# Performance work log

Hardware: AMD Instinct MI355X
Metric: run time of the kernel (lower is better)

## Reference

```python
import jax, jax.numpy as jnp
import numpy as np

DIM_IN, DIM_OUT, DIM_INNER = 1024, 1024, 128
SCALE = DIM_INNER ** -0.5


def setup_inputs() -> dict:
    key = jax.random.key(0)
    k1, k2, k3, k4 = jax.random.split(key, 4)
    x = jax.random.normal(k1, (4, 4096, DIM_IN), dtype=jnp.float32)
    # torch nn.Linear stores weight as [out, in]; we keep that layout and transpose in matmul
    w_qkv = jax.random.normal(k2, (3 * DIM_INNER, DIM_IN), dtype=jnp.float32) * (DIM_IN ** -0.5)
    w_out = jax.random.normal(k3, (DIM_OUT, DIM_INNER), dtype=jnp.float32) * (DIM_INNER ** -0.5)
    b_out = jax.random.normal(k4, (DIM_OUT,), dtype=jnp.float32) * 0.02
    return {"x": x, "w_qkv": w_qkv, "w_out": w_out, "b_out": b_out}


def reference(x, w_qkv, w_out, b_out):
    # qkv projection (no bias)
    qkv = jnp.einsum('bnd,ed->bne', x, w_qkv)            # [b, n, 3*dim_inner]
    q, k, v = jnp.split(qkv, 3, axis=-1)                 # each [b, n, dim_inner]
    sim = jnp.einsum('bid,bjd->bij', q, k) * SCALE       # [b, n, n]
    n = sim.shape[-1]
    causal = jnp.triu(jnp.ones((n, n), dtype=bool), 1)   # True above diagonal
    neg = jnp.finfo(q.dtype).max
    sim = jnp.where(causal[None, :, :], -neg, sim)
    attn = jax.nn.softmax(sim, axis=-1)
    out = jnp.einsum('bij,bjd->bid', attn, v)            # [b, n, dim_inner]
    return jnp.einsum('bnd,od->bno', out, w_out) + b_out # [b, n, dim_out]
```

## Files before the change

kernel.cpp:

```cpp
#include <hip/hip_runtime.h>
#include <math.h>


typedef __attribute__((ext_vector_type(8))) short bf16x8;
typedef __attribute__((ext_vector_type(4))) short bf16x4;
typedef __attribute__((ext_vector_type(4))) float f32x4;

#define FA_SCL2 0.12751886525137387f

__device__ __forceinline__ unsigned short f2bf(float f) {
    __bf16 h = (__bf16)f;
    return __builtin_bit_cast(unsigned short, h);
}
__device__ __forceinline__ float bf2f(unsigned short h) {
    union { unsigned u; float f; } v; v.u = ((unsigned)h) << 16;
    return v.f;
}
__device__ __forceinline__ f32x4 mfma16(bf16x8 a, bf16x8 b, f32x4 c) {
    return __builtin_amdgcn_mfma_f32_16x16x32_bf16(a, b, c, 0, 0, 0);
}
__device__ __forceinline__ void gl2lds16(const void* g, void* l) {
    __builtin_amdgcn_global_load_lds(
        (const __attribute__((address_space(1))) unsigned int*)g,
        (__attribute__((address_space(3))) unsigned int*)l, 16, 0, 0);
}
__device__ __forceinline__ f32x4 vmax4(f32x4 a, f32x4 b) {
    return f32x4{fmaxf(a[0], b[0]), fmaxf(a[1], b[1]),
                 fmaxf(a[2], b[2]), fmaxf(a[3], b[3])};
}

__global__ __launch_bounds__(256)
void wcast(const float* __restrict__ W, unsigned short* __restrict__ wfm)
{
    const int idx = blockIdx.x * 256 + threadIdx.x;
    const int kc = idx & 127, r = idx >> 7;
    const float* g = W + (size_t)r * 1024 + kc * 8;
    float4 w0 = *(const float4*)g, w1 = *(const float4*)(g + 4);
    bf16x8 p;
    p[0] = (short)f2bf(w0.x); p[1] = (short)f2bf(w0.y);
    p[2] = (short)f2bf(w0.z); p[3] = (short)f2bf(w0.w);
    p[4] = (short)f2bf(w1.x); p[5] = (short)f2bf(w1.y);
    p[6] = (short)f2bf(w1.z); p[7] = (short)f2bf(w1.w);
    *(bf16x8*)&wfm[(size_t)(kc * 384 + r) * 8] = p;
}

__global__ __launch_bounds__(256)
void woutcast(const float* __restrict__ W, unsigned short* __restrict__ wofm)
{
    const int idx = blockIdx.x * 256 + threadIdx.x;
    const int c = idx & 15, rg = idx >> 4;
    const float* g = W + (size_t)rg * 128 + c * 8;
    float4 w0 = *(const float4*)g, w1 = *(const float4*)(g + 4);
    bf16x8 p;
    p[0] = (short)f2bf(w0.x); p[1] = (short)f2bf(w0.y);
    p[2] = (short)f2bf(w0.z); p[3] = (short)f2bf(w0.w);
    p[4] = (short)f2bf(w1.x); p[5] = (short)f2bf(w1.y);
    p[6] = (short)f2bf(w1.z); p[7] = (short)f2bf(w1.w);
    *(bf16x8*)&wofm[((size_t)((rg >> 6) * 16 + c) * 64 + (rg & 63)) * 8] = p;
}

__global__ __launch_bounds__(256, 4)
void gemm_qkv(const float* __restrict__ X, const unsigned short* __restrict__ Wfm,
              unsigned short* __restrict__ qfm, unsigned short* __restrict__ kfm,
              unsigned short* __restrict__ vpl)
{
    __shared__ unsigned short Asl[2048];
    __shared__ unsigned short Bsl[3][6144];
    const int tid = threadIdx.x;
    const int wv = tid >> 6, lane = tid & 63;
    const int lm = lane & 15, quad = lane >> 4;
    const int mt = blockIdx.x & 255;
    const int nh = blockIdx.x >> 8;
    const int mb = mt * 64, nb = nh * 192;
    const int arow = tid >> 2, af4 = tid & 3;

    f32x4 acc[4][3];
    #pragma unroll
    for (int i = 0; i < 4; ++i)
        #pragma unroll
        for (int j = 0; j < 3; ++j) acc[i][j] = f32x4{0.f, 0.f, 0.f, 0.f};

    const float* gx = X + (size_t)(mb + arow) * 1024 + af4 * 8;

    auto issueB = [&](int it, int buf) {
        #pragma unroll
        for (int i = 0; i < 3; ++i) {
            const int p = wv * 3 + i;
            const int kcl = p & 3, rg = p >> 2;
            gl2lds16(Wfm + ((size_t)((it * 4 + kcl) * 384) + nb + rg * 64) * 8 + lane * 8,
                     &Bsl[buf][(kcl * 192 + rg * 64) * 8]);
        }
    };

    float4 a00 = *(const float4*)gx;
    float4 a01 = *(const float4*)(gx + 4);
    issueB(0, 0);
    float4 a10 = *(const float4*)(gx + 32);
    float4 a11 = *(const float4*)(gx + 36);
    issueB(1, 1);

    auto step = [&](const int i, float4& fa, float4& fb) {
        __builtin_amdgcn_s_barrier();
        {
            bf16x8 pk;
            pk[0] = (short)f2bf(fa.x); pk[1] = (short)f2bf(fa.y);
            pk[2] = (short)f2bf(fa.z); pk[3] = (short)f2bf(fa.w);
            pk[4] = (short)f2bf(fb.x); pk[5] = (short)f2bf(fb.y);
            pk[6] = (short)f2bf(fb.z); pk[7] = (short)f2bf(fb.w);
            *(bf16x8*)&Asl[(af4 * 64 + arow) * 8] = pk;
        }
        if (i < 30) {
            fa = *(const float4*)(gx + (i + 2) * 32);
            fb = *(const float4*)(gx + (i + 2) * 32 + 4);
            issueB(i + 2, (i + 2) % 3);
            asm volatile("s_waitcnt vmcnt(10) lgkmcnt(0)" ::: "memory");
        } else if (i == 30) {
            asm volatile("s_waitcnt vmcnt(5) lgkmcnt(0)" ::: "memory");
        } else {
            asm volatile("s_waitcnt vmcnt(0) lgkmcnt(0)" ::: "memory");
        }
        __builtin_amdgcn_s_barrier();
        const unsigned short* Bc = Bsl[i % 3];
        bf16x8 afr[4], bfr[3];
        #pragma unroll
        for (int i4 = 0; i4 < 4; ++i4)
            afr[i4] = *(const bf16x8*)&Asl[(quad * 64 + i4 * 16 + lm) * 8];
        #pragma unroll
        for (int j = 0; j < 3; ++j)
            bfr[j] = *(const bf16x8*)&Bc[(quad * 192 + wv * 48 + j * 16 + lm) * 8];
        #pragma unroll
        for (int i4 = 0; i4 < 4; ++i4)
            #pragma unroll
            for (int j = 0; j < 3; ++j)
                acc[i4][j] = mfma16(afr[i4], bfr[j], acc[i4][j]);
    };

    for (int p = 0; p < 16; ++p) { step(2 * p, a00, a01); step(2 * p + 1, a10, a11); }

    #pragma unroll
    for (int j = 0; j < 3; ++j) {
        const int ncg = nb + wv * 48 + j * 16 + lm;
        const int sect = ncg >> 7, ncol = ncg & 127;
        if (sect == 2) {
            #pragma unroll
            for (int i = 0; i < 4; ++i)
                #pragma unroll
                for (int r = 0; r < 4; ++r)
                    vpl[(size_t)(mb + i * 16 + quad * 4 + r) * 128 + ncol]
                        = f2bf(acc[i][j][r]);
        } else {
            unsigned short* dst = sect ? kfm : qfm;
            const float scl = sect ? 1.f : FA_SCL2;
            const size_t cb = ((size_t)mt * 16 + (ncol >> 3)) * 512 + (ncol & 7);
            #pragma unroll
            for (int i = 0; i < 4; ++i)
                #pragma unroll
                for (int r = 0; r < 4; ++r)
                    dst[cb + (size_t)(i * 16 + quad * 4 + r) * 8]
                        = f2bf(acc[i][j][r] * scl);
        }
    }
}

__global__ __launch_bounds__(256)
void transpose_v(const unsigned short* __restrict__ V, unsigned short* __restrict__ Vfm)
{
    __shared__ unsigned short T[128 * 72];
    const int tid = threadIdx.x;
    const int b  = blockIdx.x >> 6;
    const int kt = blockIdx.x & 63;
    const unsigned short* src = V + ((size_t)b * 4096 + kt * 64) * 128;
    #pragma unroll
    for (int i = 0; i < 4; ++i) {
        const int idx = tid + i * 256;
        const int key = idx >> 4, c8 = (idx & 15) * 8;
        bf16x8 d = *(const bf16x8*)(src + key * 128 + c8);
        #pragma unroll
        for (int e = 0; e < 8; ++e) T[(c8 + e) * 72 + key] = (unsigned short)d[e];
    }
    __syncthreads();
    unsigned short* dst = Vfm + (size_t)(b * 64 + kt) * 8192;
    #pragma unroll
    for (int i = 0; i < 4; ++i) {
        const int o = tid + i * 256;
        const int d = o & 127, c = o >> 7;
        bf16x8 x = *(const bf16x8*)&T[d * 72 + c * 8];
        *(bf16x8*)(dst + ((size_t)c * 128 + d) * 8) = x;
    }
}

__global__ __launch_bounds__(512, 4)
void flash_attn3(const unsigned short* __restrict__ Qfm, const unsigned short* __restrict__ Kfm,
                 const unsigned short* __restrict__ Vfm,
                 unsigned short* __restrict__ Opart, float* __restrict__ Ml)
{
    __shared__ unsigned short Klds[2][8192];
    __shared__ unsigned short Vlds[2][8192];
    __shared__ unsigned short Plds[8][1024];

    const int tid = threadIdx.x;
    const int wv = tid >> 6, lane = tid & 63;
    const int lm = lane & 15, quad = lane >> 4;

    const int bx = blockIdx.x;
    const int xcd = bx & 7;
    const int b   = xcd >> 1;
    const int r   = (bx >> 3) * 2 + (xcd & 1);
    const int sp  = r & 3;
    const int Qi  = (r < 64) ? (16 + (r >> 2)) : (15 - ((r - 64) >> 2));
    const int n   = 2 * Qi + 2;
    const int cnt = (n >> 2) + ((sp < (n & 3)) ? 1 : 0);
    const int ktb = sp * (n >> 2) + ((sp < (n & 3)) ? sp : (n & 3));
    const int kte = ktb + cnt;
    const int qtw = 2 * Qi + (wv >> 2);
    const int rw  = (wv & 3) * 16;

    const int qt0 = 2 * Qi;
    const size_t ob0 = (size_t)((b * 64 + qt0) * 4 + sp) * 8192;
    const size_t ob1 = ob0 + 4 * 8192;
    const int mlb0 = ((b * 64 + qt0) * 4 + sp) * 128, mlb1 = mlb0 + 512;

    if (cnt == 0) {
        bf16x8 z = {0, 0, 0, 0, 0, 0, 0, 0};
        #pragma unroll
        for (int t = 0; t < 2; ++t) {
            *(bf16x8*)&Opart[ob0 + (size_t)(tid + t * 512) * 8] = z;
            *(bf16x8*)&Opart[ob1 + (size_t)(tid + t * 512) * 8] = z;
        }
        if (tid < 64) { Ml[mlb0 + tid] = -INFINITY; Ml[mlb1 + tid] = -INFINITY; }
        else if (tid < 128) { Ml[mlb0 + tid] = 0.f; Ml[mlb1 + tid] = 0.f; }
        return;
    }

    {
        const size_t qb = (size_t)(b * 64 + qt0) * 8192;
        #pragma unroll
        for (int i = 0; i < 4; ++i) {
            const int p = wv * 4 + i;
            gl2lds16(Qfm + qb + (size_t)p * 512 + lane * 8, &Klds[0][0] + p * 512);
        }
    }
    __syncthreads();
    bf16x8 qf[4];
    {
        const unsigned short* Qt = &Klds[wv >> 2][0];
        #pragma unroll
        for (int c = 0; c < 4; ++c)
            qf[c] = *(const bf16x8*)&Qt[((c * 4 + quad) * 64 + rw + lm) * 8];
    }
    asm volatile("s_waitcnt lgkmcnt(0)" ::: "memory");
    __builtin_amdgcn_s_barrier();

    {
        const size_t kb = (size_t)(b * 64 + ktb) * 8192;
        #pragma unroll
        for (int i = 0; i < 2; ++i) {
            const int pc = wv * 2 + i;
            gl2lds16(Kfm + kb + pc * 512 + lane * 8, &Klds[0][pc * 512]);
            gl2lds16(Vfm + kb + pc * 512 + lane * 8, &Vlds[0][pc * 512]);
        }
    }

    f32x4 oacc[8];
    #pragma unroll
    for (int oc = 0; oc < 8; ++oc) oacc[oc] = f32x4{0.f, 0.f, 0.f, 0.f};
    f32x4 m4 = f32x4{-INFINITY, -INFINITY, -INFINITY, -INFINITY};
    f32x4 lacc = f32x4{0.f, 0.f, 0.f, 0.f};
    unsigned short* Pw = Plds[wv];
    const short ONE = (short)0x3F80;
    const bf16x8 ONESB = {ONE, ONE, ONE, ONE, ONE, ONE, ONE, ONE};

    for (int kt = ktb; kt < kte; ++kt) {
        const int cu = (kt - ktb) & 1;
        __builtin_amdgcn_s_barrier();
        if (kt + 1 < kte) {
            const size_t kb = (size_t)(b * 64 + kt + 1) * 8192;
            #pragma unroll
            for (int i = 0; i < 2; ++i) {
                const int pc = wv * 2 + i;
                gl2lds16(Kfm + kb + pc * 512 + lane * 8, &Klds[cu ^ 1][pc * 512]);
                gl2lds16(Vfm + kb + pc * 512 + lane * 8, &Vlds[cu ^ 1][pc * 512]);
            }
            asm volatile("s_waitcnt vmcnt(4)" ::: "memory");
        } else {
            asm volatile("s_waitcnt vmcnt(0)" ::: "memory");
        }
        __builtin_amdgcn_s_barrier();
        if (kt > qtw) continue;

        const unsigned short* Kc = &Klds[cu][0];
        const unsigned short* Vc = &Vlds[cu][0];

        f32x4 sv[4];
        __builtin_amdgcn_s_setprio(1);
        #pragma unroll
        for (int ct = 0; ct < 4; ++ct) {
            f32x4 a = f32x4{0.f, 0.f, 0.f, 0.f};
            #pragma unroll
            for (int c = 0; c < 4; ++c) {
                bf16x8 kf = *(const bf16x8*)&Kc[((c * 4 + quad) * 64 + ct * 16 + lm) * 8];
                a = mfma16(qf[c], kf, a);
            }
            sv[ct] = a;
        }
        __builtin_amdgcn_s_setprio(0);
        if (kt == qtw) {
            #pragma unroll
            for (int ct = 0; ct < 4; ++ct) {
                const int dg = ct * 16 + lm - rw - quad * 4;
                #pragma unroll
                for (int rr = 0; rr < 4; ++rr)
                    if (dg > rr) sv[ct][rr] = -INFINITY;
            }
        }
        const f32x4 pmax = vmax4(vmax4(sv[0], sv[1]), vmax4(sv[2], sv[3]));
        const float dm = fmaxf(fmaxf(pmax[0] - m4[0], pmax[1] - m4[1]),
                               fmaxf(pmax[2] - m4[2], pmax[3] - m4[3]));
        if (!__all(dm <= 8.f)) {
            f32x4 rmax = pmax;
            #pragma unroll
            for (int d = 1; d < 16; d <<= 1) {
                f32x4 o;
                #pragma unroll
                for (int e = 0; e < 4; ++e) o[e] = __shfl_xor(rmax[e], d);
                rmax = vmax4(rmax, o);
            }
            const f32x4 mnew = vmax4(m4, rmax);
            f32x4 alpha;
            #pragma unroll
            for (int e = 0; e < 4; ++e) alpha[e] = __builtin_amdgcn_exp2f(m4[e] - mnew[e]);
            m4 = mnew;
            #pragma unroll
            for (int oc = 0; oc < 8; ++oc) oacc[oc] *= alpha;
            lacc *= alpha;
        }
        #pragma unroll
        for (int ct = 0; ct < 4; ++ct)
            #pragma unroll
            for (int rr = 0; rr < 4; ++rr)
                sv[ct][rr] = __builtin_amdgcn_exp2f(sv[ct][rr] - m4[rr]);
        #pragma unroll
        for (int ct = 0; ct < 4; ++ct) {
            const int cb = ((ct * 2 + (lm >> 3)) * 16 + quad * 4) * 8 + (lm & 7);
            #pragma unroll
            for (int rr = 0; rr < 4; ++rr)
                Pw[cb + rr * 8] = f2bf(sv[ct][rr]);
        }
        __builtin_amdgcn_s_setprio(1);
        #pragma unroll
        for (int s = 0; s < 2; ++s) {
            bf16x8 pf = *(const bf16x8*)&Pw[((s * 4 + quad) * 16 + lm) * 8];
            lacc = mfma16(pf, ONESB, lacc);
            #pragma unroll
            for (int oc = 0; oc < 8; ++oc) {
                bf16x8 vf = *(const bf16x8*)&Vc[((s * 4 + quad) * 128 + oc * 16 + lm) * 8];
                oacc[oc] = mfma16(pf, vf, oacc[oc]);
            }
        }
        __builtin_amdgcn_s_setprio(0);
    }

    const size_t obw = (size_t)((b * 64 + qtw) * 4 + sp) * 8192;
    const int mlw = ((b * 64 + qtw) * 4 + sp) * 128;
    #pragma unroll
    for (int oc = 0; oc < 8; ++oc) {
        const size_t cb = obw + (size_t)((oc * 2 + (lm >> 3)) * 64
                          + rw + quad * 4) * 8 + (lm & 7);
        #pragma unroll
        for (int rr = 0; rr < 4; ++rr)
            Opart[cb + rr * 8] = f2bf(oacc[oc][rr]);
    }
    if (lm == 0)
        #pragma unroll
        for (int rr = 0; rr < 4; ++rr) {
            const int row = rw + quad * 4 + rr;
            Ml[mlw + row] = m4[rr];
            Ml[mlw + 64 + row] = lacc[rr];
        }
}

__global__ __launch_bounds__(256)
void fa_combine(const unsigned short* __restrict__ Opart, const float* __restrict__ Ml,
                unsigned short* __restrict__ Ofm)
{
    const int bq = blockIdx.x;
    const int tid = threadIdx.x;
    const size_t pbase = (size_t)bq * 4 * 8192;
    const int mlb = bq * 4 * 128;
    #pragma unroll
    for (int t = 0; t < 4; ++t) {
        const int g = tid + t * 256;
        const int r = g & 63;
        float m[4], l[4];
        #pragma unroll
        for (int s = 0; s < 4; ++s) {
            m[s] = Ml[mlb + s * 128 + r];
            l[s] = Ml[mlb + s * 128 + 64 + r];
        }
        const float M = fmaxf(fmaxf(m[0], m[1]), fmaxf(m[2], m[3]));
        float a[4], den = 0.f;
        #pragma unroll
        for (int s = 0; s < 4; ++s) {
            a[s] = __builtin_amdgcn_exp2f(m[s] - M);
            den += a[s] * l[s];
        }
        const float rsc = 1.f / den;
        float acc[8] = {};
        #pragma unroll
        for (int s = 0; s < 4; ++s) {
            bf16x8 x = *(const bf16x8*)&Opart[pbase + (size_t)s * 8192 + (size_t)g * 8];
            #pragma unroll
            for (int e = 0; e < 8; ++e) acc[e] += a[s] * bf2f((unsigned short)x[e]);
        }
        bf16x8 o;
        #pragma unroll
        for (int e = 0; e < 8; ++e) o[e] = f2bf(acc[e] * rsc);
        *(bf16x8*)&Ofm[(size_t)bq * 8192 + (size_t)g * 8] = o;
    }
}

__global__ __launch_bounds__(256, 4)
void gemm_out(const unsigned short* __restrict__ Ain, const unsigned short* __restrict__ Wofm,
              const float* __restrict__ bias, float* __restrict__ out)
{
    __shared__ unsigned short Bsl[16384];
    __shared__ unsigned short Asl[2][4096];
    const int tid = threadIdx.x;
    const int mb = blockIdx.x * 128;
    const int nb = blockIdx.y * 128;
    const int wv = tid >> 6, lane = tid & 63;
    const int wr = (wv >> 1) * 64, wc = (wv & 1) * 64;
    const int lm = lane & 15, quad = lane >> 4;

    #pragma unroll
    for (int i = 0; i < 8; ++i) {
        const int p = wv * 8 + i;
        gl2lds16(Wofm + (size_t)(((nb >> 6) + (p >> 4)) * 16 + (p & 15)) * 512 + lane * 8,
                 &Bsl[p * 512]);
    }
    #pragma unroll
    for (int i = 0; i < 2; ++i) {
        const int id = wv * 2 + i, t = id >> 2, kcl = id & 3;
        gl2lds16(Ain + (size_t)((mb >> 6) + t) * 8192 + kcl * 512 + lane * 8,
                 &Asl[0][(t * 4 + kcl) * 512]);
    }

    f32x4 acc[4][4];
    #pragma unroll
    for (int i = 0; i < 4; ++i)
        #pragma unroll
        for (int j = 0; j < 4; ++j) acc[i][j] = f32x4{0.f, 0.f, 0.f, 0.f};

    for (int kt = 0; kt < 4; ++kt) {
        __builtin_amdgcn_s_barrier();
        if (kt < 3) {
            #pragma unroll
            for (int i = 0; i < 2; ++i) {
                const int id = wv * 2 + i, t = id >> 2, kcl = id & 3;
                gl2lds16(Ain + (size_t)((mb >> 6) + t) * 8192 + ((kt + 1) * 4 + kcl) * 512 + lane * 8,
                         &Asl[(kt + 1) & 1][(t * 4 + kcl) * 512]);
            }
            asm volatile("s_waitcnt vmcnt(2)" ::: "memory");
        } else {
            asm volatile("s_waitcnt vmcnt(0)" ::: "memory");
        }
        __builtin_amdgcn_s_barrier();
        const unsigned short* Ac = Asl[kt & 1];
        bf16x8 af[4], bfr[4];
        #pragma unroll
        for (int i = 0; i < 4; ++i)
            af[i] = *(const bf16x8*)&Ac[(((wv >> 1) * 4 + quad) * 64 + i * 16 + lm) * 8];
        #pragma unroll
        for (int j = 0; j < 4; ++j)
            bfr[j] = *(const bf16x8*)&Bsl[(((wc >> 6) * 16 + kt * 4 + quad) * 64 + j * 16 + lm) * 8];
        #pragma unroll
        for (int i = 0; i < 4; ++i)
            #pragma unroll
            for (int j = 0; j < 4; ++j)
                acc[i][j] = mfma16(af[i], bfr[j], acc[i][j]);
    }

    #pragma unroll
    for (int j = 0; j < 4; ++j) {
        const int col = nb + wc + j * 16 + lm;
        const float bv = bias[col];
        #pragma unroll
        for (int i = 0; i < 4; ++i)
            #pragma unroll
            for (int r = 0; r < 4; ++r) {
                const int m = mb + wr + i * 16 + quad * 4 + r;
                out[(size_t)m * 1024 + col] = acc[i][j][r] + bv;
            }
    }
}

extern "C" void kernel_launch(void* const* d_in, const int* in_sizes, int n_in,
                              void* d_out, int out_size, void* d_ws, size_t ws_size,
                              hipStream_t stream)
{
    (void)in_sizes; (void)n_in; (void)out_size; (void)ws_size;
    const float* x     = (const float*)d_in[0];
    const float* w_qkv = (const float*)d_in[1];
    const float* w_out = (const float*)d_in[2];
    const float* b_out = (const float*)d_in[3];
    float* out = (float*)d_out;
    unsigned short* ws = (unsigned short*)d_ws;

    const size_t NE = (size_t)16384 * 128;
    unsigned short* qfm = ws;
    unsigned short* kfm = ws + NE;
    unsigned short* vpl = ws + 2 * NE;
    unsigned short* vfm = ws + 3 * NE;
    unsigned short* op  = ws + 4 * NE;
    float*          ml  = (float*)(ws + 8 * NE);
    unsigned short* ofm = qfm;
    unsigned short* wfm = op;
    unsigned short* wofm = vpl;

    hipLaunchKernelGGL(wcast,       dim3(192),    dim3(256), 0, stream, w_qkv, wfm);
    hipLaunchKernelGGL(gemm_qkv,    dim3(512),    dim3(256), 0, stream, x, wfm, qfm, kfm, vpl);
    hipLaunchKernelGGL(transpose_v, dim3(256),    dim3(256), 0, stream, vpl, vfm);
    hipLaunchKernelGGL(woutcast,    dim3(64),     dim3(256), 0, stream, w_out, wofm);
    hipLaunchKernelGGL(flash_attn3, dim3(512),    dim3(512), 0, stream, qfm, kfm, vfm, op, ml);
    hipLaunchKernelGGL(fa_combine,  dim3(256),    dim3(256), 0, stream, op, ml, ofm);
    hipLaunchKernelGGL(gemm_out,    dim3(128, 8), dim3(256), 0, stream, ofm, wofm, b_out, out);
}
```

Measured before the change: 196.2 us.

## Retile QKV projection GEMM to 64x128 tiles with K=64 steps and double buffering

Restructures the QKV GEMM from 64x192 tiles over K=32 steps with triple-buffered B into 64x128 tiles over K=64 steps with double-buffered B. Each wave now computes a 2x4 block of 16x16 MFMA tiles, using a 2x2 wave grid instead of splitting only along N. The grid grows to 768 blocks, so each block writes exactly one of Q, K or V. The aim is fewer barriers per unit of work and more parallel blocks. In exchange, X is re-read from global memory three times instead of twice, and the occupancy hint drops to 3 blocks per CU.

New measurement: 203.2 us. +3.5%, slower.

```diff
diff --git a/kernel.cpp b/kernel.cpp
--- a/kernel.cpp
+++ b/kernel.cpp
@@ -59,106 +59,130 @@
     *(bf16x8*)&wofm[((size_t)((rg >> 6) * 16 + c) * 64 + (rg & 63)) * 8] = p;
 }
 
-__global__ __launch_bounds__(256, 4)
+__global__ __launch_bounds__(256, 3)
 void gemm_qkv(const float* __restrict__ X, const unsigned short* __restrict__ Wfm,
               unsigned short* __restrict__ qfm, unsigned short* __restrict__ kfm,
               unsigned short* __restrict__ vpl)
 {
-    __shared__ unsigned short Asl[2048];
-    __shared__ unsigned short Bsl[3][6144];
+    __shared__ unsigned short Asl[4096];
+    __shared__ unsigned short Bsl[2][8192];
     const int tid = threadIdx.x;
     const int wv = tid >> 6, lane = tid & 63;
     const int lm = lane & 15, quad = lane >> 4;
     const int mt = blockIdx.x & 255;
-    const int nh = blockIdx.x >> 8;
-    const int mb = mt * 64, nb = nh * 192;
-    const int arow = tid >> 2, af4 = tid & 3;
-
-    f32x4 acc[4][3];
-    #pragma unroll
-    for (int i = 0; i < 4; ++i)
-        #pragma unroll
-        for (int j = 0; j < 3; ++j) acc[i][j] = f32x4{0.f, 0.f, 0.f, 0.f};
-
-    const float* gx = X + (size_t)(mb + arow) * 1024 + af4 * 8;
-
+    const int nt = blockIdx.x >> 8;
+    const int mb = mt * 64, nb = nt * 128;
+    const int wr = wv >> 1, wc = wv & 1;
+
+    const int kc0 = tid >> 6, rowA = tid & 63;
+    const float* gxr = X + (size_t)(mb + rowA) * 1024;
+
+    f32x4 acc[2][4];
+    #pragma unroll
+    for (int i = 0; i < 2; ++i)
+        #pragma unroll
+        for (int j = 0; j < 4; ++j) acc[i][j] = f32x4{0.f, 0.f, 0.f, 0.f};
+
+    auto loadA = [&](int it, float4& r0, float4& r1, float4& r2, float4& r3) {
+        const float* g = gxr + it * 64;
+        r0 = *(const float4*)(g + kc0 * 8);
+        r1 = *(const float4*)(g + kc0 * 8 + 4);
+        r2 = *(const float4*)(g + (kc0 + 4) * 8);
+        r3 = *(const float4*)(g + (kc0 + 4) * 8 + 4);
+    };
+    auto stageA = [&](const float4& r0, const float4& r1,
+                      const float4& r2, const float4& r3) {
+        bf16x8 p0, p1;
+        p0[0] = (short)f2bf(r0.x); p0[1] = (short)f2bf(r0.y);
+        p0[2] = (short)f2bf(r0.z); p0[3] = (short)f2bf(r0.w);
+        p0[4] = (short)f2bf(r1.x); p0[5] = (short)f2bf(r1.y);
+        p0[6] = (short)f2bf(r1.z); p0[7] = (short)f2bf(r1.w);
+        *(bf16x8*)&Asl[tid * 8] = p0;
+        p1[0] = (short)f2bf(r2.x); p1[1] = (short)f2bf(r2.y);
+        p1[2] = (short)f2bf(r2.z); p1[3] = (short)f2bf(r2.w);
+        p1[4] = (short)f2bf(r3.x); p1[5] = (short)f2bf(r3.y);
+        p1[6] = (short)f2bf(r3.z); p1[7] = (short)f2bf(r3.w);
+        *(bf16x8*)&Asl[(tid + 256) * 8] = p1;
+    };
     auto issueB = [&](int it, int buf) {
         #pragma unroll
-        for (int i = 0; i < 3; ++i) {
-            const int p = wv * 3 + i;
-            const int kcl = p & 3, rg = p >> 2;
-            gl2lds16(Wfm + ((size_t)((it * 4 + kcl) * 384) + nb + rg * 64) * 8 + lane * 8,
-                     &Bsl[buf][(kcl * 192 + rg * 64) * 8]);
+        for (int i = 0; i < 4; ++i) {
+            const int p = wv * 4 + i;
+            const int kc = p >> 1, colh = (p & 1) * 64;
+            gl2lds16(Wfm + ((size_t)(it * 8 + kc) * 384 + nb + colh + lane) * 8,
+                     &Bsl[buf][(kc * 128 + colh) * 8]);
         }
     };
 
-    float4 a00 = *(const float4*)gx;
-    float4 a01 = *(const float4*)(gx + 4);
+    float4 a0, a1, a2, a3, b0, b1, b2, b3;
+    loadA(0, a0, a1, a2, a3);
     issueB(0, 0);
-    float4 a10 = *(const float4*)(gx + 32);
-    float4 a11 = *(const float4*)(gx + 36);
-    issueB(1, 1);
-
-    auto step = [&](const int i, float4& fa, float4& fb) {
+    loadA(1, b0, b1, b2, b3);
+
+    auto step = [&](const int i, float4& r0, float4& r1, float4& r2, float4& r3) {
         __builtin_amdgcn_s_barrier();
-        {
-            bf16x8 pk;
-            pk[0] = (short)f2bf(fa.x); pk[1] = (short)f2bf(fa.y);
-            pk[2] = (short)f2bf(fa.z); pk[3] = (short)f2bf(fa.w);
-            pk[4] = (short)f2bf(fb.x); pk[5] = (short)f2bf(fb.y);
-            pk[6] = (short)f2bf(fb.z); pk[7] = (short)f2bf(fb.w);
-            *(bf16x8*)&Asl[(af4 * 64 + arow) * 8] = pk;
-        }
-        if (i < 30) {
-            fa = *(const float4*)(gx + (i + 2) * 32);
-            fb = *(const float4*)(gx + (i + 2) * 32 + 4);
-            issueB(i + 2, (i + 2) % 3);
-            asm volatile("s_waitcnt vmcnt(10) lgkmcnt(0)" ::: "memory");
-        } else if (i == 30) {
-            asm volatile("s_waitcnt vmcnt(5) lgkmcnt(0)" ::: "memory");
+        stageA(r0, r1, r2, r3);
+        if (i < 15) issueB(i + 1, (i + 1) & 1);
+        if (i < 14) {
+            loadA(i + 2, r0, r1, r2, r3);
+            asm volatile("s_waitcnt vmcnt(12) lgkmcnt(0)" ::: "memory");
+        } else if (i == 14) {
+            asm volatile("s_waitcnt vmcnt(8) lgkmcnt(0)" ::: "memory");
         } else {
             asm volatile("s_waitcnt vmcnt(0) lgkmcnt(0)" ::: "memory");
         }
         __builtin_amdgcn_s_barrier();
-        const unsigned short* Bc = Bsl[i % 3];
-        bf16x8 afr[4], bfr[3];
-        #pragma unroll
-        for (int i4 = 0; i4 < 4; ++i4)
-            afr[i4] = *(const bf16x8*)&Asl[(quad * 64 + i4 * 16 + lm) * 8];
-        #pragma unroll
-        for (int j = 0; j < 3; ++j)
-            bfr[j] = *(const bf16x8*)&Bc[(quad * 192 + wv * 48 + j * 16 + lm) * 8];
-        #pragma unroll
-        for (int i4 = 0; i4 < 4; ++i4)
-            #pragma unroll
-            for (int j = 0; j < 3; ++j)
-                acc[i4][j] = mfma16(afr[i4], bfr[j], acc[i4][j]);
+        const unsigned short* Bc = Bsl[i & 1];
+        bf16x8 af[2][2], bfr[2][4];
+        #pragma unroll
+        for (int s = 0; s < 2; ++s) {
+            const int kc = s * 4 + quad;
+            #pragma unroll
+            for (int ii = 0; ii < 2; ++ii)
+                af[s][ii] = *(const bf16x8*)&Asl[(kc * 64 + wr * 32 + ii * 16 + lm) * 8];
+            #pragma unroll
+            for (int j = 0; j < 4; ++j)
+                bfr[s][j] = *(const bf16x8*)&Bc[(kc * 128 + wc * 64 + j * 16 + lm) * 8];
+        }
+        #pragma unroll
+        for (int s = 0; s < 2; ++s)
+            #pragma unroll
+            for (int ii = 0; ii < 2; ++ii)
+                #pragma unroll
+                for (int j = 0; j < 4; ++j)
+                    acc[ii][j] = mfma16(af[s][ii], bfr[s][j], acc[ii][j]);
     };
 
-    for (int p = 0; p < 16; ++p) { step(2 * p, a00, a01); step(2 * p + 1, a10, a11); }
-
-    #pragma unroll
-    for (int j = 0; j < 3; ++j) {
-        const int ncg = nb + wv * 48 + j * 16 + lm;
-        const int sect = ncg >> 7, ncol = ncg & 127;
-        if (sect == 2) {
-            #pragma unroll
-            for (int i = 0; i < 4; ++i)
+    for (int p = 0; p < 8; ++p) {
+        step(2 * p,     a0, a1, a2, a3);
+        step(2 * p + 1, b0, b1, b2, b3);
+    }
+
+    if (nt == 2) {
+        #pragma unroll
+        for (int ii = 0; ii < 2; ++ii)
+            #pragma unroll
+            for (int j = 0; j < 4; ++j) {
+                const int ncol = wc * 64 + j * 16 + lm;
                 #pragma unroll
                 for (int r = 0; r < 4; ++r)
-                    vpl[(size_t)(mb + i * 16 + quad * 4 + r) * 128 + ncol]
-                        = f2bf(acc[i][j][r]);
-        } else {
-            unsigned short* dst = sect ? kfm : qfm;
-            const float scl = sect ? 1.f : FA_SCL2;
-            const size_t cb = ((size_t)mt * 16 + (ncol >> 3)) * 512 + (ncol & 7);
-            #pragma unroll
-            for (int i = 0; i < 4; ++i)
+                    vpl[(size_t)(mb + wr * 32 + ii * 16 + quad * 4 + r) * 128 + ncol]
+                        = f2bf(acc[ii][j][r]);
+            }
+    } else {
+        unsigned short* dst = nt ? kfm : qfm;
+        const float scl = nt ? 1.f : FA_SCL2;
+        #pragma unroll
+        for (int ii = 0; ii < 2; ++ii)
+            #pragma unroll
+            for (int j = 0; j < 4; ++j) {
+                const int ncol = wc * 64 + j * 16 + lm;
+                const size_t cb = ((size_t)mt * 16 + (ncol >> 3)) * 512 + (ncol & 7);
                 #pragma unroll
                 for (int r = 0; r < 4; ++r)
-                    dst[cb + (size_t)(i * 16 + quad * 4 + r) * 8]
-                        = f2bf(acc[i][j][r] * scl);
-        }
+                    dst[cb + (size_t)(wr * 32 + ii * 16 + quad * 4 + r) * 8]
+                        = f2bf(acc[ii][j][r] * scl);
+            }
     }
 }
 
@@ -518,7 +542,7 @@
     unsigned short* wofm = vpl;
 
     hipLaunchKernelGGL(wcast,       dim3(192),    dim3(256), 0, stream, w_qkv, wfm);
-    hipLaunchKernelGGL(gemm_qkv,    dim3(512),    dim3(256), 0, stream, x, wfm, qfm, kfm, vpl);
+    hipLaunchKernelGGL(gemm_qkv,    dim3(768),    dim3(256), 0, stream, x, wfm, qfm, kfm, vpl);
     hipLaunchKernelGGL(transpose_v, dim3(256),    dim3(256), 0, stream, vpl, vfm);
     hipLaunchKernelGGL(woutcast,    dim3(64),     dim3(256), 0, stream, w_out, wofm);
     hipLaunchKernelGGL(flash_attn3, dim3(512),    dim3(512), 0, stream, qfm, kfm, vfm, op, ml);
```
